# Kernel tuning notes

Hardware: AMD Instinct MI355X
Metric: run time of the kernel (lower is better)

## Reference

```python
import jax, jax.numpy as jnp
import numpy as np

NUM_USERS = 200000
NUM_PRODUCTS = 100000
N_NODES = NUM_USERS + NUM_PRODUCTS
N_EDGES = 1000000
USER_FDIM = 128
PROD_FDIM = 128
EDIM = 64


def setup_inputs() -> dict:
    key = jax.random.key(0)
    ks = jax.random.split(key, 16)
    s = 0.02
    inp = {
        "edge_index": jnp.stack([
            jax.random.randint(ks[0], (N_EDGES,), 0, NUM_USERS, dtype=jnp.int32).astype(jnp.int64),
            jax.random.randint(ks[1], (N_EDGES,), 0, NUM_PRODUCTS, dtype=jnp.int32).astype(jnp.int64),
        ], axis=0),
        "user_features": jax.random.normal(ks[2], (NUM_USERS, USER_FDIM), jnp.float32),
        "product_features": jax.random.normal(ks[3], (NUM_PRODUCTS, PROD_FDIM), jnp.float32),
        "user_emb": jax.random.normal(ks[4], (NUM_USERS, EDIM), jnp.float32) * s,
        "product_emb": jax.random.normal(ks[5], (NUM_PRODUCTS, EDIM), jnp.float32) * s,
        "W_uf": jax.random.normal(ks[6], (USER_FDIM, EDIM), jnp.float32) * s,
        "b_uf": jnp.zeros((EDIM,), jnp.float32),
        "W_pf": jax.random.normal(ks[7], (PROD_FDIM, EDIM), jnp.float32) * s,
        "b_pf": jnp.zeros((EDIM,), jnp.float32),
        "conv1_W": jax.random.normal(ks[8], (EDIM, EDIM), jnp.float32) * s,
        "conv1_b": jnp.zeros((EDIM,), jnp.float32),
        "conv2_W": jax.random.normal(ks[9], (EDIM, EDIM), jnp.float32) * s,
        "conv2_b": jnp.zeros((EDIM,), jnp.float32),
        "pred_W1": jax.random.normal(ks[10], (2 * EDIM, EDIM), jnp.float32) * s,
        "pred_b1": jnp.zeros((EDIM,), jnp.float32),
        "pred_W2": jax.random.normal(ks[11], (EDIM, 1), jnp.float32) * s,
        "pred_b2": jnp.zeros((1,), jnp.float32),
    }
    return inp


def _gcn_conv(x, W, b, row, col, n_nodes):
    # PyG GCNConv: h = x W; out[col] += deg^-1/2[row] * deg^-1/2[col] * h[row]; + b
    h = x @ W
    deg = jax.ops.segment_sum(jnp.ones_like(col, dtype=x.dtype), col, num_segments=n_nodes)
    dis = jnp.where(deg > 0, jax.lax.rsqrt(jnp.maximum(deg, 1.0)), 0.0)
    norm = dis[row] * dis[col]                     # [E_total]
    msgs = h[row] * norm[:, None]                  # gather + edge weight
    out = jax.ops.segment_sum(msgs, col, num_segments=n_nodes)  # scatter-add
    return out + b


def reference(edge_index, user_features, product_features, user_emb, product_emb,
              W_uf, b_uf, W_pf, b_pf, conv1_W, conv1_b, conv2_W, conv2_b,
              pred_W1, pred_b1, pred_W2, pred_b2):
    user_idx = edge_index[0]
    prod_idx = edge_index[1]

    user_x = user_features @ W_uf + b_uf + user_emb          # [Nu, D]
    prod_x = product_features @ W_pf + b_pf + product_emb    # [Np, D]
    x = jnp.concatenate([user_x, prod_x], axis=0)            # [N, D]

    # symmetrized edges + self-loops (GCNConv default add_self_loops=True)
    ar = jnp.arange(N_NODES, dtype=edge_index.dtype)
    row = jnp.concatenate([user_idx, prod_idx, ar])
    col = jnp.concatenate([prod_idx, user_idx, ar])

    x = jax.nn.relu(_gcn_conv(x, conv1_W, conv1_b, row, col, N_NODES))
    # dropout p=0.2 is identity in eval mode
    x = _gcn_conv(x, conv2_W, conv2_b, row, col, N_NODES)

    user_e = x[:NUM_USERS][user_idx]                          # [E, D]
    prod_e = x[NUM_USERS:][prod_idx]                          # [E, D]
    pair = jnp.concatenate([user_e, prod_e], axis=1)          # [E, 2D]
    h = jax.nn.relu(pair @ pred_W1 + pred_b1)
    logits = h @ pred_W2 + pred_b2                            # [E, 1]
    preds = jax.nn.sigmoid(logits).squeeze(-1) * 5.0
    return preds
```

## Files before the change

### kernel.cpp

```cpp
#include <hip/hip_runtime.h>
#include <math.h>

#define NUM_USERS 200000
#define NUM_PRODUCTS 100000
#define N_NODES 300000
#define N_EDGES 1000000
#define EDIM 64
#define FDIM 128
#define CAP 40
#define LDST 72
#define NT_U 12500
#define NT_ALL 18750
#define ZERO_BLK 1173
#define NBUK 80
#define BNODES 2500
#define BINCAP 49152
#define CSR_REP 4

typedef __attribute__((ext_vector_type(8))) short short8;
typedef __attribute__((ext_vector_type(4))) float f32x4;

static __device__ inline short f2bf(float f) {
    unsigned int u = __float_as_uint(f);
    unsigned int r = (u + 0x7FFFu + ((u >> 16) & 1u)) >> 16;
    return (short)r;
}
static __device__ inline float bf2f(unsigned short s) {
    return __uint_as_float(((unsigned int)s) << 16);
}
static __device__ inline float disf(int c) {
    return rsqrtf(1.0f + (float)c);
}

__global__ void k_setup(int* __restrict__ cnt,
                        const float* __restrict__ W_uf, const float* __restrict__ W_pf,
                        const float* __restrict__ c1, const float* __restrict__ c2,
                        const float* __restrict__ W1, short* __restrict__ wts) {
    int b = blockIdx.x;
    if (b < ZERO_BLK) {
        int i = b * 256 + threadIdx.x;
        if (i < 300032 + NBUK) cnt[i] = 0;
        return;
    }
    int gid = (b - ZERO_BLK) * 256 + threadIdx.x;
    if (gid >= 32768) return;
    if (gid < 8192) {
        int n = gid >> 7, k = gid & 127;
        wts[gid] = f2bf(W_uf[k * 64 + n]);
    } else if (gid < 16384) {
        int i = gid - 8192; int n = i >> 7, k = i & 127;
        wts[gid] = f2bf(W_pf[k * 64 + n]);
    } else if (gid < 20480) {
        int i = gid - 16384; int n = i >> 6, k = i & 63;
        wts[gid] = f2bf(c1[k * 64 + n]);
    } else if (gid < 24576) {
        int i = gid - 20480; int n = i >> 6, k = i & 63;
        wts[gid] = f2bf(c2[k * 64 + n]);
    } else {
        int i = gid - 24576; int n = i >> 7, k = i & 127;
        wts[gid] = f2bf(W1[k * 64 + n]);
    }
}

__global__ __launch_bounds__(256) void k_bin(
    const int* __restrict__ ei, int* __restrict__ gcnt, int* __restrict__ gbin) {
    __shared__ int lcnt[NBUK];
    __shared__ int lbase[NBUK];
    int tid = threadIdx.x;
    if (tid < NBUK) lcnt[tid] = 0;
    __syncthreads();
    int e0 = (blockIdx.x * 256 + tid) * 4;
    bool act = e0 < N_EDGES;
    int d[8], s[8], rk[8], bk[8];
    if (act) {
        int4 uu = *(const int4*)(ei + e0);
        int4 pp = *(const int4*)(ei + N_EDGES + e0);
        d[0] = pp.x; s[0] = uu.x;  d[1] = uu.x; s[1] = pp.x;
        d[2] = pp.y; s[2] = uu.y;  d[3] = uu.y; s[3] = pp.y;
        d[4] = pp.z; s[4] = uu.z;  d[5] = uu.z; s[5] = pp.z;
        d[6] = pp.w; s[6] = uu.w;  d[7] = uu.w; s[7] = pp.w;
#pragma unroll
        for (int j = 0; j < 8; ++j) {
            bk[j] = d[j] / BNODES;
            rk[j] = atomicAdd(&lcnt[bk[j]], 1);
        }
    }
    __syncthreads();
    if (tid < NBUK) lbase[tid] = atomicAdd(&gcnt[tid], lcnt[tid]);
    __syncthreads();
    if (act) {
#pragma unroll
        for (int j = 0; j < 8; ++j) {
            int pos = lbase[bk[j]] + rk[j];
            if (pos < BINCAP)
                *(int2*)(gbin + ((size_t)bk[j] * BINCAP + pos) * 2) = make_int2(d[j], s[j]);
        }
    }
}

__global__ __launch_bounds__(256) void k_csr(
    const int* __restrict__ gcnt, const int* __restrict__ gbin,
    int* __restrict__ cnt, int* __restrict__ adj) {
    int i = blockIdx.x;
    int xcd = i & 7, k = i >> 3;
    int bucket = (k % (NBUK / 8)) * 8 + xcd;
    int rep = k / (NBUK / 8);
    int n = gcnt[bucket];
    const int* bb = gbin + (size_t)bucket * BINCAP * 2;
    const int stride = CSR_REP * 256;
    int idx = rep * 256 + threadIdx.x;
    for (; idx + 3 * stride < n; idx += 4 * stride) {
        int2 e0 = *(const int2*)(bb + (size_t)(idx)*2);
        int2 e1 = *(const int2*)(bb + (size_t)(idx + stride) * 2);
        int2 e2 = *(const int2*)(bb + (size_t)(idx + 2 * stride) * 2);
        int2 e3 = *(const int2*)(bb + (size_t)(idx + 3 * stride) * 2);
        int s0 = atomicAdd(&cnt[e0.x], 1);
        int s1 = atomicAdd(&cnt[e1.x], 1);
        int s2 = atomicAdd(&cnt[e2.x], 1);
        int s3 = atomicAdd(&cnt[e3.x], 1);
        adj[(size_t)e0.x * CAP + s0] = e0.y;
        adj[(size_t)e1.x * CAP + s1] = e1.y;
        adj[(size_t)e2.x * CAP + s2] = e2.y;
        adj[(size_t)e3.x * CAP + s3] = e3.y;
    }
    for (; idx < n; idx += stride) {
        int2 e = *(const int2*)(bb + (size_t)idx * 2);
        int s = atomicAdd(&cnt[e.x], 1);
        adj[(size_t)e.x * CAP + s] = e.y;
    }
}

__global__ __launch_bounds__(256) void k_xform_c1(
    const float* __restrict__ user_feat, const float* __restrict__ prod_feat,
    const short* __restrict__ wts,
    const float* __restrict__ b_uf, const float* __restrict__ b_pf,
    const float* __restrict__ user_emb, const float* __restrict__ prod_emb,
    const int* __restrict__ cnt, unsigned short* __restrict__ h) {
    __shared__ unsigned short lds[4][16 * LDST];
    int tid = threadIdx.x;
    int wave = tid >> 6;
    int tile = blockIdx.x * 4 + wave;
    if (tile >= NT_ALL) tile = NT_ALL - 1;
    int lane = tid & 63, ln = lane & 15, quad = lane >> 4;

    const float* feat; const short* WT; const float* b; const float* emb;
    int node_off, mtile;
    if (tile < NT_U) {
        feat = user_feat; WT = wts;        b = b_uf; emb = user_emb; node_off = 0;         mtile = tile;
    } else {
        feat = prod_feat; WT = wts + 8192; b = b_pf; emb = prod_emb; node_off = NUM_USERS; mtile = tile - NT_U;
    }
    const short* c1T = wts + 16384;

    short8 Bx[4][4];
#pragma unroll
    for (int t = 0; t < 4; ++t)
#pragma unroll
        for (int kk = 0; kk < 4; ++kk)
            Bx[t][kk] = *(const short8*)(WT + ((t * 16 + ln) * 128 + kk * 32 + quad * 8));
    short8 Bc[4][2];
#pragma unroll
    for (int t = 0; t < 4; ++t)
#pragma unroll
        for (int kk = 0; kk < 2; ++kk)
            Bc[t][kk] = *(const short8*)(c1T + ((t * 16 + ln) * 64 + kk * 32 + quad * 8));
    float bv[4];
#pragma unroll
    for (int t = 0; t < 4; ++t) bv[t] = b[t * 16 + ln];

    int mbase = mtile * 16;
    const float* arow = feat + (size_t)(mbase + ln) * FDIM + quad * 8;

    f32x4 acc[4] = {{0.f,0.f,0.f,0.f},{0.f,0.f,0.f,0.f},{0.f,0.f,0.f,0.f},{0.f,0.f,0.f,0.f}};
#pragma unroll
    for (int kk = 0; kk < 4; ++kk) {
        float4 lo = *(const float4*)(arow + kk * 32);
        float4 hi = *(const float4*)(arow + kk * 32 + 4);
        short8 Af;
        Af[0] = f2bf(lo.x); Af[1] = f2bf(lo.y); Af[2] = f2bf(lo.z); Af[3] = f2bf(lo.w);
        Af[4] = f2bf(hi.x); Af[5] = f2bf(hi.y); Af[6] = f2bf(hi.z); Af[7] = f2bf(hi.w);
#pragma unroll
        for (int t = 0; t < 4; ++t)
            acc[t] = __builtin_amdgcn_mfma_f32_16x16x32_bf16(Af, Bx[t][kk], acc[t], 0, 0, 0);
    }
#pragma unroll
    for (int r = 0; r < 4; ++r) {
        int node = mbase + quad * 4 + r;
#pragma unroll
        for (int t = 0; t < 4; ++t) {
            float v = acc[t][r] + bv[t] + emb[(size_t)node * EDIM + t * 16 + ln];
            lds[wave][(quad * 4 + r) * LDST + t * 16 + ln] = (unsigned short)f2bf(v);
        }
    }
    __syncthreads();
    f32x4 acch[4] = {{0.f,0.f,0.f,0.f},{0.f,0.f,0.f,0.f},{0.f,0.f,0.f,0.f},{0.f,0.f,0.f,0.f}};
#pragma unroll
    for (int kk = 0; kk < 2; ++kk) {
        short8 Af = *(const short8*)(&lds[wave][ln * LDST + kk * 32 + quad * 8]);
#pragma unroll
        for (int t = 0; t < 4; ++t)
            acch[t] = __builtin_amdgcn_mfma_f32_16x16x32_bf16(Af, Bc[t][kk], acch[t], 0, 0, 0);
    }
    float disv[4];
#pragma unroll
    for (int r = 0; r < 4; ++r) disv[r] = disf(cnt[node_off + mbase + quad * 4 + r]);
#pragma unroll
    for (int r = 0; r < 4; ++r) {
        int node = mbase + quad * 4 + r;
#pragma unroll
        for (int t = 0; t < 4; ++t)
            h[(size_t)(node_off + node) * EDIM + t * 16 + ln] =
                (unsigned short)f2bf(disv[r] * acch[t][r]);
    }
}

__global__ __launch_bounds__(256) void k_gather_c2(
    const int* __restrict__ adj, const int* __restrict__ cnt,
    const unsigned short* __restrict__ h,
    const float* __restrict__ b1, const short* __restrict__ c2T,
    unsigned short* __restrict__ hout) {
    __shared__ unsigned short lds[4][16 * LDST];
    int tid = threadIdx.x;
    int wave = tid >> 6;
    int tile = blockIdx.x * 4 + wave;
    if (tile >= N_NODES / 16) tile = N_NODES / 16 - 1;
    int lane = tid & 63, ln = lane & 15, quad = lane >> 4;
    const unsigned int* hp = (const unsigned int*)h;

    short8 Bc[4][2];
#pragma unroll
    for (int t = 0; t < 4; ++t)
#pragma unroll
        for (int kk = 0; kk < 2; ++kk)
            Bc[t][kk] = *(const short8*)(c2T + ((t * 16 + ln) * 64 + kk * 32 + quad * 8));

    int mbase = tile * 16;
    float2 bb0 = ((const float2*)b1)[ln];
    float2 bb1 = ((const float2*)b1)[16 + ln];

#pragma unroll 1
    for (int it = 0; it < 4; ++it) {
        int d = mbase + it * 4 + quad;
        const unsigned int* hrow = hp + (size_t)d * 32;
        unsigned int s0 = hrow[ln], s1 = hrow[16 + ln];
        float a0 = bf2f((unsigned short)s0);
        float a1 = bf2f((unsigned short)(s0 >> 16));
        float a2 = bf2f((unsigned short)s1);
        float a3 = bf2f((unsigned short)(s1 >> 16));
        int cd = cnt[d];
        const int* ap = adj + (size_t)d * CAP;
        int i = 0;
        for (; i + 1 < cd; i += 2) {
            int r0 = ap[i], r1 = ap[i + 1];
            unsigned int p00 = hp[(size_t)r0 * 32 + ln];
            unsigned int p01 = hp[(size_t)r0 * 32 + 16 + ln];
            unsigned int p10 = hp[(size_t)r1 * 32 + ln];
            unsigned int p11 = hp[(size_t)r1 * 32 + 16 + ln];
            a0 += bf2f((unsigned short)p00) + bf2f((unsigned short)p10);
            a1 += bf2f((unsigned short)(p00 >> 16)) + bf2f((unsigned short)(p10 >> 16));
            a2 += bf2f((unsigned short)p01) + bf2f((unsigned short)p11);
            a3 += bf2f((unsigned short)(p01 >> 16)) + bf2f((unsigned short)(p11 >> 16));
        }
        if (i < cd) {
            int r0 = ap[i];
            unsigned int p00 = hp[(size_t)r0 * 32 + ln];
            unsigned int p01 = hp[(size_t)r0 * 32 + 16 + ln];
            a0 += bf2f((unsigned short)p00);
            a1 += bf2f((unsigned short)(p00 >> 16));
            a2 += bf2f((unsigned short)p01);
            a3 += bf2f((unsigned short)(p01 >> 16));
        }
        float dv = disf(cd);
        float v0 = fmaxf(fmaf(dv, a0, bb0.x), 0.f);
        float v1 = fmaxf(fmaf(dv, a1, bb0.y), 0.f);
        float v2 = fmaxf(fmaf(dv, a2, bb1.x), 0.f);
        float v3 = fmaxf(fmaf(dv, a3, bb1.y), 0.f);
        unsigned int* lrow = (unsigned int*)&lds[wave][(it * 4 + quad) * LDST];
        lrow[ln] = ((unsigned int)(unsigned short)f2bf(v1) << 16)
                 | (unsigned int)(unsigned short)f2bf(v0);
        lrow[16 + ln] = ((unsigned int)(unsigned short)f2bf(v3) << 16)
                      | (unsigned int)(unsigned short)f2bf(v2);
    }
    __syncthreads();
    f32x4 acc[4] = {{0.f,0.f,0.f,0.f},{0.f,0.f,0.f,0.f},{0.f,0.f,0.f,0.f},{0.f,0.f,0.f,0.f}};
#pragma unroll
    for (int kk = 0; kk < 2; ++kk) {
        short8 Af = *(const short8*)(&lds[wave][ln * LDST + kk * 32 + quad * 8]);
#pragma unroll
        for (int t = 0; t < 4; ++t)
            acc[t] = __builtin_amdgcn_mfma_f32_16x16x32_bf16(Af, Bc[t][kk], acc[t], 0, 0, 0);
    }
    float disv[4];
#pragma unroll
    for (int r = 0; r < 4; ++r) disv[r] = disf(cnt[mbase + quad * 4 + r]);
#pragma unroll
    for (int r = 0; r < 4; ++r) {
        int node = mbase + quad * 4 + r;
#pragma unroll
        for (int t = 0; t < 4; ++t)
            hout[(size_t)node * EDIM + t * 16 + ln] = (unsigned short)f2bf(disv[r] * acc[t][r]);
    }
}

__global__ __launch_bounds__(256) void k_gather(
    const int* __restrict__ adj, const int* __restrict__ cnt,
    const unsigned short* __restrict__ h,
    const float* __restrict__ b, unsigned short* __restrict__ xout, int relu) {
    int d = blockIdx.x * 4 + (threadIdx.x >> 6);
    if (d >= N_NODES) return;
    int l = threadIdx.x & 63;
    int half = l >> 5, c2 = l & 31;
    const unsigned int* hp = (const unsigned int*)h;

    float ax = 0.f, ay = 0.f;
    if (half == 0) {
        unsigned int pr = hp[(size_t)d * 32 + c2];
        ax = bf2f((unsigned short)pr);
        ay = bf2f((unsigned short)(pr >> 16));
    }
    int c = cnt[d];
    const int* ap = adj + (size_t)d * CAP;
    int i = 0;
    for (; i + 3 < c; i += 4) {
        int s0 = ap[i + half];
        int s1 = ap[i + 2 + half];
        unsigned int p0 = hp[(size_t)s0 * 32 + c2];
        unsigned int p1 = hp[(size_t)s1 * 32 + c2];
        ax += bf2f((unsigned short)p0) + bf2f((unsigned short)p1);
        ay += bf2f((unsigned short)(p0 >> 16)) + bf2f((unsigned short)(p1 >> 16));
    }
    if (i + half < c) {
        unsigned int p0 = hp[(size_t)ap[i + half] * 32 + c2];
        ax += bf2f((unsigned short)p0);
        ay += bf2f((unsigned short)(p0 >> 16));
    }
    if (i + 2 + half < c) {
        unsigned int p0 = hp[(size_t)ap[i + 2 + half] * 32 + c2];
        ax += bf2f((unsigned short)p0);
        ay += bf2f((unsigned short)(p0 >> 16));
    }
    ax += __shfl_xor(ax, 32, 64);
    ay += __shfl_xor(ay, 32, 64);
    float dv = disf(c);
    float2 bb = ((const float2*)b)[c2];
    float v0 = fmaf(dv, ax, bb.x);
    float v1 = fmaf(dv, ay, bb.y);
    if (relu) { v0 = fmaxf(v0, 0.f); v1 = fmaxf(v1, 0.f); }
    if (half == 0) {
        unsigned int pk = ((unsigned int)(unsigned short)f2bf(v1) << 16)
                        | (unsigned int)(unsigned short)f2bf(v0);
        ((unsigned int*)xout)[(size_t)d * 32 + c2] = pk;
    }
}

__global__ __launch_bounds__(256) void k_pred_mfma(
    const int* __restrict__ ei, const unsigned short* __restrict__ x,
    const short* __restrict__ W1T, const float* __restrict__ b1,
    const float* __restrict__ W2, const float* __restrict__ b2,
    float* __restrict__ preds) {
    int tid = threadIdx.x;
    int wave = tid >> 6, lane = tid & 63;
    int ln = lane & 15, quad = lane >> 4;

    short8 Bf[4][4];
#pragma unroll
    for (int t = 0; t < 4; ++t)
#pragma unroll
        for (int kk = 0; kk < 4; ++kk)
            Bf[t][kk] = *(const short8*)(W1T + ((t * 16 + ln) * 128 + kk * 32 + quad * 8));

    float b1v[4], W2v[4];
#pragma unroll
    for (int t = 0; t < 4; ++t) {
        b1v[t] = b1[t * 16 + ln];
        W2v[t] = W2[t * 16 + ln];
    }
    float b2s = b2[0];

    const int n_tiles = N_EDGES / 16;
    int gw = blockIdx.x * 4 + wave;
    int nwaves = gridDim.x * 4;

    int cu = 0, cp = 0;
    if (gw < n_tiles) {
        cu = ei[gw * 16 + ln];
        cp = ei[N_EDGES + gw * 16 + ln] + NUM_USERS;
    }
    for (int tile = gw; tile < n_tiles; tile += nwaves) {
        int u = cu, p = cp;
        int nt = tile + nwaves;
        if (nt < n_tiles) {
            cu = ei[nt * 16 + ln];
            cp = ei[N_EDGES + nt * 16 + ln] + NUM_USERS;
        }
        short8 Af[4];
        Af[0] = *(const short8*)(x + (size_t)u * EDIM + quad * 8);
        Af[1] = *(const short8*)(x + (size_t)u * EDIM + 32 + quad * 8);
        Af[2] = *(const short8*)(x + (size_t)p * EDIM + quad * 8);
        Af[3] = *(const short8*)(x + (size_t)p * EDIM + 32 + quad * 8);

        f32x4 acc[4] = {{0.f,0.f,0.f,0.f},{0.f,0.f,0.f,0.f},{0.f,0.f,0.f,0.f},{0.f,0.f,0.f,0.f}};
#pragma unroll
        for (int kk = 0; kk < 4; ++kk)
#pragma unroll
            for (int t = 0; t < 4; ++t)
                acc[t] = __builtin_amdgcn_mfma_f32_16x16x32_bf16(Af[kk], Bf[t][kk], acc[t], 0, 0, 0);

        float out[4];
#pragma unroll
        for (int r = 0; r < 4; ++r) {
            float part = 0.f;
#pragma unroll
            for (int t = 0; t < 4; ++t) {
                float hv = fmaxf(acc[t][r] + b1v[t], 0.f);
                part = fmaf(hv, W2v[t], part);
            }
            part += __shfl_xor(part, 1, 64);
            part += __shfl_xor(part, 2, 64);
            part += __shfl_xor(part, 4, 64);
            part += __shfl_xor(part, 8, 64);
            out[r] = part;
        }
        if (ln == 0) {
            int ebase = tile * 16;
#pragma unroll
            for (int r = 0; r < 4; ++r) {
                float logit = out[r] + b2s;
                preds[ebase + quad * 4 + r] = 5.f / (1.f + expf(-logit));
            }
        }
    }
}

extern "C" void kernel_launch(void* const* d_in, const int* in_sizes, int n_in,
                              void* d_out, int out_size, void* d_ws, size_t ws_size,
                              hipStream_t stream) {
    const int*   ei        = (const int*)d_in[0];
    const float* user_feat = (const float*)d_in[1];
    const float* prod_feat = (const float*)d_in[2];
    const float* user_emb  = (const float*)d_in[3];
    const float* prod_emb  = (const float*)d_in[4];
    const float* W_uf      = (const float*)d_in[5];
    const float* b_uf      = (const float*)d_in[6];
    const float* W_pf      = (const float*)d_in[7];
    const float* b_pf      = (const float*)d_in[8];
    const float* conv1_W   = (const float*)d_in[9];
    const float* conv1_b   = (const float*)d_in[10];
    const float* conv2_W   = (const float*)d_in[11];
    const float* conv2_b   = (const float*)d_in[12];
    const float* pred_W1   = (const float*)d_in[13];
    const float* pred_b1   = (const float*)d_in[14];
    const float* pred_W2   = (const float*)d_in[15];
    const float* pred_b2   = (const float*)d_in[16];

    int* ws_i = (int*)d_ws;
    int*   cnt  = ws_i;
    int*   gcnt = ws_i + 300032;
    int*   adj  = ws_i + 600064;
    unsigned short* xbuf = (unsigned short*)(ws_i + 12601344);
    int*   gbin = ws_i + 12601344;
    unsigned short* hbuf = (unsigned short*)(ws_i + 22201344);
    short* wts = (short*)(ws_i + 31801344);
    float* preds = (float*)d_out;

    k_setup<<<ZERO_BLK + 128, 256, 0, stream>>>(cnt, W_uf, W_pf, conv1_W, conv2_W, pred_W1, wts);
    k_bin<<<(N_EDGES / 4 + 255) / 256, 256, 0, stream>>>(ei, gcnt, gbin);
    k_csr<<<NBUK * CSR_REP, 256, 0, stream>>>(gcnt, gbin, cnt, adj);

    k_xform_c1<<<(NT_ALL + 3) / 4, 256, 0, stream>>>(user_feat, prod_feat, wts,
                                                     b_uf, b_pf, user_emb, prod_emb,
                                                     cnt, hbuf);

    k_gather_c2<<<(18750 + 3) / 4, 256, 0, stream>>>(adj, cnt, hbuf, conv1_b,
                                                     wts + 20480, xbuf);
    k_gather<<<N_NODES / 4, 256, 0, stream>>>(adj, cnt, xbuf, conv2_b, hbuf, 0);

    k_pred_mfma<<<2048, 256, 0, stream>>>(ei, hbuf, wts + 24576, pred_b1, pred_W2, pred_b2, preds);
}
```

Baseline: 681.6 us.

## Persistent double-buffered feature transform and drop per-wave block barriers

After: 670.6 us. No clear change (-1.6%).

```diff
diff --git a/kernel.cpp b/kernel.cpp
--- a/kernel.cpp
+++ b/kernel.cpp
@@ -10,12 +10,16 @@
 #define CAP 40
 #define LDST 72
 #define NT_U 12500
+#define NT_P 6250
 #define NT_ALL 18750
 #define ZERO_BLK 1173
 #define NBUK 80
 #define BNODES 2500
 #define BINCAP 49152
 #define CSR_REP 4
+#define XC1_BLOCKS 1024
+#define XC1_WAVES (XC1_BLOCKS * 4)
+#define XC1_UW 2731
 
 typedef __attribute__((ext_vector_type(8))) short short8;
 typedef __attribute__((ext_vector_type(4))) float f32x4;
@@ -130,7 +134,65 @@
     }
 }
 
-__global__ __launch_bounds__(256) void k_xform_c1(
+#define XC1_LOAD(S, MT) do {                                                         \
+    int mb_ = (MT) * 16;                                                             \
+    const float* ar_ = feat + (size_t)(mb_ + ln) * FDIM + quad * 8;                  \
+    _Pragma("unroll")                                                                \
+    for (int kk_ = 0; kk_ < 4; ++kk_) {                                              \
+        fl##S[kk_] = *(const float4*)(ar_ + kk_ * 32);                               \
+        fh##S[kk_] = *(const float4*)(ar_ + kk_ * 32 + 4);                           \
+    }                                                                                \
+    _Pragma("unroll")                                                                \
+    for (int r_ = 0; r_ < 4; ++r_)                                                   \
+        _Pragma("unroll")                                                            \
+        for (int t_ = 0; t_ < 4; ++t_)                                               \
+            ev##S[r_][t_] = emb[(size_t)(mb_ + quad * 4 + r_) * EDIM + t_ * 16 + ln];\
+    _Pragma("unroll")                                                                \
+    for (int r_ = 0; r_ < 4; ++r_)                                                   \
+        cd##S[r_] = cnt[node_off + mb_ + quad * 4 + r_];                             \
+} while (0)
+
+#define XC1_COMPUTE(S, MT) do {                                                      \
+    int mb_ = (MT) * 16;                                                             \
+    f32x4 acc_[4] = {{0.f,0.f,0.f,0.f},{0.f,0.f,0.f,0.f},{0.f,0.f,0.f,0.f},{0.f,0.f,0.f,0.f}}; \
+    _Pragma("unroll")                                                                \
+    for (int kk_ = 0; kk_ < 4; ++kk_) {                                              \
+        short8 Af_;                                                                  \
+        Af_[0] = f2bf(fl##S[kk_].x); Af_[1] = f2bf(fl##S[kk_].y);                    \
+        Af_[2] = f2bf(fl##S[kk_].z); Af_[3] = f2bf(fl##S[kk_].w);                    \
+        Af_[4] = f2bf(fh##S[kk_].x); Af_[5] = f2bf(fh##S[kk_].y);                    \
+        Af_[6] = f2bf(fh##S[kk_].z); Af_[7] = f2bf(fh##S[kk_].w);                    \
+        _Pragma("unroll")                                                            \
+        for (int t_ = 0; t_ < 4; ++t_)                                               \
+            acc_[t_] = __builtin_amdgcn_mfma_f32_16x16x32_bf16(Af_, Bx[t_][kk_], acc_[t_], 0, 0, 0); \
+    }                                                                                \
+    _Pragma("unroll")                                                                \
+    for (int r_ = 0; r_ < 4; ++r_)                                                   \
+        _Pragma("unroll")                                                            \
+        for (int t_ = 0; t_ < 4; ++t_) {                                             \
+            float v_ = acc_[t_][r_] + bv[t_] + ev##S[r_][t_];                        \
+            lds[wave][(quad * 4 + r_) * LDST + t_ * 16 + ln] = (unsigned short)f2bf(v_); \
+        }                                                                            \
+    f32x4 acch_[4] = {{0.f,0.f,0.f,0.f},{0.f,0.f,0.f,0.f},{0.f,0.f,0.f,0.f},{0.f,0.f,0.f,0.f}}; \
+    _Pragma("unroll")                                                                \
+    for (int kk_ = 0; kk_ < 2; ++kk_) {                                              \
+        short8 Af_ = *(const short8*)(&lds[wave][ln * LDST + kk_ * 32 + quad * 8]);  \
+        _Pragma("unroll")                                                            \
+        for (int t_ = 0; t_ < 4; ++t_)                                               \
+            acch_[t_] = __builtin_amdgcn_mfma_f32_16x16x32_bf16(Af_, Bc[t_][kk_], acch_[t_], 0, 0, 0); \
+    }                                                                                \
+    _Pragma("unroll")                                                                \
+    for (int r_ = 0; r_ < 4; ++r_) {                                                 \
+        float dv_ = disf(cd##S[r_]);                                                 \
+        int node_ = mb_ + quad * 4 + r_;                                             \
+        _Pragma("unroll")                                                            \
+        for (int t_ = 0; t_ < 4; ++t_)                                               \
+            h[(size_t)(node_off + node_) * EDIM + t_ * 16 + ln] =                    \
+                (unsigned short)f2bf(dv_ * acch_[t_][r_]);                           \
+    }                                                                                \
+} while (0)
+
+__global__ __launch_bounds__(256, 2) void k_xform_c1(
     const float* __restrict__ user_feat, const float* __restrict__ prod_feat,
     const short* __restrict__ wts,
     const float* __restrict__ b_uf, const float* __restrict__ b_pf,
@@ -139,17 +201,19 @@
     __shared__ unsigned short lds[4][16 * LDST];
     int tid = threadIdx.x;
     int wave = tid >> 6;
-    int tile = blockIdx.x * 4 + wave;
-    if (tile >= NT_ALL) tile = NT_ALL - 1;
     int lane = tid & 63, ln = lane & 15, quad = lane >> 4;
+    int gw = blockIdx.x * 4 + wave;
 
     const float* feat; const short* WT; const float* b; const float* emb;
-    int node_off, mtile;
-    if (tile < NT_U) {
-        feat = user_feat; WT = wts;        b = b_uf; emb = user_emb; node_off = 0;         mtile = tile;
+    int node_off, t0, tcnt, tstride;
+    if (gw < XC1_UW) {
+        feat = user_feat; WT = wts;        b = b_uf; emb = user_emb;
+        node_off = 0;         t0 = gw;          tcnt = NT_U; tstride = XC1_UW;
     } else {
-        feat = prod_feat; WT = wts + 8192; b = b_pf; emb = prod_emb; node_off = NUM_USERS; mtile = tile - NT_U;
-    }
+        feat = prod_feat; WT = wts + 8192; b = b_pf; emb = prod_emb;
+        node_off = NUM_USERS; t0 = gw - XC1_UW; tcnt = NT_P; tstride = XC1_WAVES - XC1_UW;
+    }
+    if (t0 >= tcnt) return;
     const short* c1T = wts + 16384;
 
     short8 Bx[4][4];
@@ -168,49 +232,25 @@
 #pragma unroll
     for (int t = 0; t < 4; ++t) bv[t] = b[t * 16 + ln];
 
-    int mbase = mtile * 16;
-    const float* arow = feat + (size_t)(mbase + ln) * FDIM + quad * 8;
-
-    f32x4 acc[4] = {{0.f,0.f,0.f,0.f},{0.f,0.f,0.f,0.f},{0.f,0.f,0.f,0.f},{0.f,0.f,0.f,0.f}};
-#pragma unroll
-    for (int kk = 0; kk < 4; ++kk) {
-        float4 lo = *(const float4*)(arow + kk * 32);
-        float4 hi = *(const float4*)(arow + kk * 32 + 4);
-        short8 Af;
-        Af[0] = f2bf(lo.x); Af[1] = f2bf(lo.y); Af[2] = f2bf(lo.z); Af[3] = f2bf(lo.w);
-        Af[4] = f2bf(hi.x); Af[5] = f2bf(hi.y); Af[6] = f2bf(hi.z); Af[7] = f2bf(hi.w);
-#pragma unroll
-        for (int t = 0; t < 4; ++t)
-            acc[t] = __builtin_amdgcn_mfma_f32_16x16x32_bf16(Af, Bx[t][kk], acc[t], 0, 0, 0);
-    }
-#pragma unroll
-    for (int r = 0; r < 4; ++r) {
-        int node = mbase + quad * 4 + r;
-#pragma unroll
-        for (int t = 0; t < 4; ++t) {
-            float v = acc[t][r] + bv[t] + emb[(size_t)node * EDIM + t * 16 + ln];
-            lds[wave][(quad * 4 + r) * LDST + t * 16 + ln] = (unsigned short)f2bf(v);
-        }
-    }
-    __syncthreads();
-    f32x4 acch[4] = {{0.f,0.f,0.f,0.f},{0.f,0.f,0.f,0.f},{0.f,0.f,0.f,0.f},{0.f,0.f,0.f,0.f}};
-#pragma unroll
-    for (int kk = 0; kk < 2; ++kk) {
-        short8 Af = *(const short8*)(&lds[wave][ln * LDST + kk * 32 + quad * 8]);
-#pragma unroll
-        for (int t = 0; t < 4; ++t)
-            acch[t] = __builtin_amdgcn_mfma_f32_16x16x32_bf16(Af, Bc[t][kk], acch[t], 0, 0, 0);
-    }
-    float disv[4];
-#pragma unroll
-    for (int r = 0; r < 4; ++r) disv[r] = disf(cnt[node_off + mbase + quad * 4 + r]);
-#pragma unroll
-    for (int r = 0; r < 4; ++r) {
-        int node = mbase + quad * 4 + r;
-#pragma unroll
-        for (int t = 0; t < 4; ++t)
-            h[(size_t)(node_off + node) * EDIM + t * 16 + ln] =
-                (unsigned short)f2bf(disv[r] * acch[t][r]);
+    float4 flA[4], fhA[4], flB[4], fhB[4];
+    float evA[4][4], evB[4][4];
+    int cdA[4], cdB[4];
+
+    int t = t0;
+    XC1_LOAD(A, t);
+    for (;;) {
+        int tn = t + tstride;
+        bool hasB = tn < tcnt;
+        if (hasB) XC1_LOAD(B, tn);
+        XC1_COMPUTE(A, t);
+        if (!hasB) break;
+        t = tn;
+        tn = t + tstride;
+        bool hasA = tn < tcnt;
+        if (hasA) XC1_LOAD(A, tn);
+        XC1_COMPUTE(B, t);
+        if (!hasA) break;
+        t = tn;
     }
 }
 
@@ -223,7 +263,7 @@
     int tid = threadIdx.x;
     int wave = tid >> 6;
     int tile = blockIdx.x * 4 + wave;
-    if (tile >= N_NODES / 16) tile = N_NODES / 16 - 1;
+    if (tile >= N_NODES / 16) return;
     int lane = tid & 63, ln = lane & 15, quad = lane >> 4;
     const unsigned int* hp = (const unsigned int*)h;
 
@@ -281,7 +321,6 @@
         lrow[16 + ln] = ((unsigned int)(unsigned short)f2bf(v3) << 16)
                       | (unsigned int)(unsigned short)f2bf(v2);
     }
-    __syncthreads();
     f32x4 acc[4] = {{0.f,0.f,0.f,0.f},{0.f,0.f,0.f,0.f},{0.f,0.f,0.f,0.f},{0.f,0.f,0.f,0.f}};
 #pragma unroll
     for (int kk = 0; kk < 2; ++kk) {
@@ -467,9 +506,9 @@
     k_bin<<<(N_EDGES / 4 + 255) / 256, 256, 0, stream>>>(ei, gcnt, gbin);
     k_csr<<<NBUK * CSR_REP, 256, 0, stream>>>(gcnt, gbin, cnt, adj);
 
-    k_xform_c1<<<(NT_ALL + 3) / 4, 256, 0, stream>>>(user_feat, prod_feat, wts,
-                                                     b_uf, b_pf, user_emb, prod_emb,
-                                                     cnt, hbuf);
+    k_xform_c1<<<XC1_BLOCKS, 256, 0, stream>>>(user_feat, prod_feat, wts,
+                                               b_uf, b_pf, user_emb, prod_emb,
+                                               cnt, hbuf);
 
     k_gather_c2<<<(18750 + 3) / 4, 256, 0, stream>>>(adj, cnt, hbuf, conv1_b,
                                                      wts + 20480, xbuf);
```
